# Performance work log

Measured on AMD Instinct MI355X. Metric: run time of the kernel, lower is better.

## Reference

```python
import jax, jax.numpy as jnp
import numpy as np

B, K, N, D, L = 16, 16, 1024, 256, 8
LN_EPS = 1e-5


def setup_inputs() -> dict:
    key = jax.random.key(0)
    ks = jax.random.split(key, 12)
    w = lambda k, sh: jax.random.normal(k, sh, jnp.float32) * 0.02
    return {
        "H": jax.random.normal(ks[0], (B, K, N, D), jnp.float32),
        "eps": jax.random.normal(ks[1], (B, L, D), jnp.float32),  # single Gaussian draw per batch
        "mu": jnp.zeros((1, L, D), jnp.float32),
        "log_sigma": jnp.full((1, L, D), -2.0, jnp.float32),
        "Wq": w(ks[2], (D, D)), "bq": jnp.zeros((D,), jnp.float32),
        "Wk": w(ks[3], (D, D)), "bk": jnp.zeros((D,), jnp.float32),
        "Wv": w(ks[4], (D, D)), "bv": jnp.zeros((D,), jnp.float32),
        "W_ih": w(ks[5], (3 * D, D)), "b_ih": jnp.zeros((3 * D,), jnp.float32),
        "W_hh": w(ks[6], (3 * D, D)), "b_hh": jnp.zeros((3 * D,), jnp.float32),
        "W1": w(ks[7], (D, D)), "b1": jnp.zeros((D,), jnp.float32),
        "W2": w(ks[8], (D, D)), "b2": jnp.zeros((D,), jnp.float32),
        "ln_g": jnp.ones((D,), jnp.float32), "ln_b": jnp.zeros((D,), jnp.float32),
    }


def reference(H, eps, mu, log_sigma, Wq, bq, Wk, bk, Wv, bv,
              W_ih, b_ih, W_hh, b_hh, W1, b1, W2, b2, ln_g, ln_b):
    d = H.shape[-1]
    scale = 1.0 / jnp.sqrt(jnp.asarray(d, H.dtype))
    slots0 = mu + jnp.exp(log_sigma) * eps  # [B,L,D]

    def step(slots, h_t):  # slots [B,L,D], h_t [B,N,D]
        Q = slots @ Wq.T + bq
        Kt = h_t @ Wk.T + bk
        V = h_t @ Wv.T + bv
        scores = jnp.einsum("bld,bnd->bln", Q, Kt) * scale
        attn = jnp.nan_to_num(jax.nn.softmax(scores, axis=-1))
        upd = jnp.einsum("bln,bnd->bld", attn, V)
        # torch.nn.GRUCell(input=upd, hidden=slots)
        gi = upd @ W_ih.T + b_ih
        gh = slots @ W_hh.T + b_hh
        ir, iz, inn = jnp.split(gi, 3, axis=-1)
        hr, hz, hn = jnp.split(gh, 3, axis=-1)
        r = jax.nn.sigmoid(ir + hr)
        z = jax.nn.sigmoid(iz + hz)
        n = jnp.tanh(inn + r * hn)
        s2 = (1.0 - z) * n + z * slots
        # FFN + residual + LayerNorm
        ffn = jnp.maximum(s2 @ W1.T + b1, 0.0) @ W2.T + b2
        x = s2 + ffn
        mean = x.mean(axis=-1, keepdims=True)
        var = x.var(axis=-1, keepdims=True)
        s3 = (x - mean) / jnp.sqrt(var + LN_EPS) * ln_g + ln_b
        return s3, (s3, attn)

    _, (S, Beta) = jax.lax.scan(step, slots0, jnp.swapaxes(H, 0, 1))
    return jnp.swapaxes(S, 0, 1), jnp.swapaxes(Beta, 0, 1)  # [B,K,L,D], [B,K,L,N]
```

## Files before the change

### kernel.cpp

```cpp
#include <hip/hip_runtime.h>
#include <math.h>


#define Bn 16
#define KK 16
#define Nn 1024
#define Dn 256
#define Ln 8

#define OFF_WQK   0
#define OFF_BQK   65536
#define OFF_WGIT  65792
#define OFF_BGI   262400
#define OFF_WHHT  263168
#define OFF_W1T   459776
#define OFF_W2T   525312
#define OFF_SLOTS 590848
#define OFF_QK    623616
#define OFF_PAV   656384
#define OFF_PDEN  1704960

__device__ __forceinline__ float sigmoidf_(float x) { return 1.f / (1.f + __expf(-x)); }

__global__ __launch_bounds__(256) void p1_kernel(
    const float* __restrict__ Wq, const float* __restrict__ bq,
    const float* __restrict__ Wk, float* __restrict__ Wqk, float* __restrict__ bqk) {
  int w = blockIdx.x, tid = threadIdx.x;
  if (w < 256) {
    float acc = 0.f;
    for (int a = 0; a < 256; ++a) acc += Wq[a * 256 + w] * Wk[a * 256 + tid];
    Wqk[w * 256 + tid] = acc;
  } else {
    float acc = 0.f;
    for (int a = 0; a < 256; ++a) acc += bq[a] * Wk[a * 256 + tid];
    bqk[tid] = acc;
  }
}

__global__ __launch_bounds__(256) void p2_kernel(
    const float* __restrict__ Wih, const float* __restrict__ bih,
    const float* __restrict__ Wv, const float* __restrict__ bv,
    float* __restrict__ WgiT, float* __restrict__ bgi) {
  int d = blockIdx.x, tid = threadIdx.x;
  float a0 = 0.f, a1 = 0.f, a2 = 0.f;
  for (int c = 0; c < 256; ++c) {
    float wv = Wv[c * 256 + d];
    a0 += Wih[tid * 256 + c] * wv;
    a1 += Wih[(tid + 256) * 256 + c] * wv;
    a2 += Wih[(tid + 512) * 256 + c] * wv;
  }
  WgiT[d * 768 + tid] = a0;
  WgiT[d * 768 + 256 + tid] = a1;
  WgiT[d * 768 + 512 + tid] = a2;
  if (d < 3) {
    int jj = d * 256 + tid;
    float s = bih[jj];
    for (int c = 0; c < 256; ++c) s += Wih[jj * 256 + c] * bv[c];
    bgi[jj] = s;
  }
}

__global__ __launch_bounds__(256) void p3_kernel(
    const float* __restrict__ Whh, const float* __restrict__ W1,
    const float* __restrict__ W2, float* __restrict__ WhhT,
    float* __restrict__ W1T, float* __restrict__ W2T) {
  __shared__ float tile[32][33];
  int wg = blockIdx.x, tid = threadIdx.x;
  const float* in; float* out; int R, C, tr, tc;
  if (wg < 192)      { in = Whh; out = WhhT; R = 768; C = 256; wg -= 0;   tr = wg >> 3; tc = wg & 7; }
  else if (wg < 256) { in = W1;  out = W1T;  R = 256; C = 256; wg -= 192; tr = wg >> 3; tc = wg & 7; }
  else               { in = W2;  out = W2T;  R = 256; C = 256; wg -= 256; tr = wg >> 3; tc = wg & 7; }
  int r = tid >> 5, c = tid & 31;
#pragma unroll
  for (int k = 0; k < 4; ++k)
    tile[r + 8 * k][c] = in[(tr * 32 + r + 8 * k) * C + tc * 32 + c];
  __syncthreads();
#pragma unroll
  for (int k = 0; k < 4; ++k)
    out[(tc * 32 + r + 8 * k) * R + tr * 32 + c] = tile[c][r + 8 * k];
}

__global__ __launch_bounds__(256) void init_slots_kernel(
    const float* __restrict__ eps, const float* __restrict__ mu,
    const float* __restrict__ lsig, float* __restrict__ slots) {
  int idx = blockIdx.x * 256 + threadIdx.x;
  int r = idx & 2047;
  slots[idx] = mu[r] + expf(lsig[r]) * eps[idx];
}

__global__ __launch_bounds__(256) void qk0_kernel(
    const float* __restrict__ Wqk, const float* __restrict__ bqk,
    const float* __restrict__ slots, float* __restrict__ Qkout) {
  __shared__ float sl_s[2048];
  int j = blockIdx.x & 7, b = blockIdx.x >> 3, tid = threadIdx.x;
  for (int k = 0; k < 8; ++k) sl_s[tid + k * 256] = slots[b * 2048 + tid + k * 256];
  __syncthreads();
  int l = tid >> 5, ee = j * 32 + (tid & 31);
  float acc = bqk[ee];
  for (int d = 0; d < 256; ++d) acc += sl_s[l * 256 + d] * Wqk[d * 256 + ee];
  Qkout[b * 2048 + l * 256 + ee] = acc;
}

__global__ __launch_bounds__(256) void attn_kernel(
    const float* __restrict__ H, const float* __restrict__ Qk,
    float* __restrict__ beta_out, float* __restrict__ par_av,
    float* __restrict__ par_den, int t) {
  __shared__ float h_s[32 * 258];
  __shared__ float qk_s[Ln * Dn];
  __shared__ float e_s[256];
  __shared__ float red[256];
  int tile = blockIdx.x, b = blockIdx.y, tid = threadIdx.x;
#pragma unroll
  for (int k = 0; k < 8; ++k) qk_s[tid + k * 256] = Qk[b * 2048 + tid + k * 256];
  const float* Hbase = H + (((long)b * KK + t) * Nn + tile * 32) * Dn;
  const float4* src = (const float4*)Hbase;
#pragma unroll
  for (int k = 0; k < 8; ++k) {
    int idx4 = tid + k * 256;
    int r = idx4 >> 6, d4 = idx4 & 63;
    float4 v = src[idx4];
    float* dst = &h_s[r * 258 + d4 * 4];
    ((float2*)dst)[0] = make_float2(v.x, v.y);
    ((float2*)dst)[1] = make_float2(v.z, v.w);
  }
  __syncthreads();
  int l = tid >> 5, row = tid & 31;
  {
    const float2* hr2 = (const float2*)(&h_s[row * 258]);
    const float2* qr2 = (const float2*)(&qk_s[l * 256]);
    float acc = 0.f;
#pragma unroll 8
    for (int e = 0; e < 128; ++e) {
      float2 hv = hr2[e], qv = qr2[e];
      acc += hv.x * qv.x + hv.y * qv.y;
    }
    float ev = __expf(acc * 0.0625f);
    e_s[tid] = ev;
    red[tid] = ev;
    beta_out[(((long)b * KK + t) * Ln + l) * Nn + tile * 32 + row] = ev;
  }
  __syncthreads();
  if (tid < 8) {
    float s = 0.f;
    for (int i = 0; i < 32; ++i) s += red[tid * 32 + i];
    par_den[(b * 32 + tile) * 8 + tid] = s;
  }
  float av[8];
#pragma unroll
  for (int i = 0; i < 8; ++i) av[i] = 0.f;
  for (int rr = 0; rr < 32; ++rr) {
    float hv = h_s[rr * 258 + tid];
#pragma unroll
    for (int i = 0; i < 8; ++i) av[i] += e_s[i * 32 + rr] * hv;
  }
  long pbase = (long)(b * 32 + tile) * 2048;
#pragma unroll
  for (int i = 0; i < 8; ++i) par_av[pbase + i * 256 + tid] = av[i];
}

__global__ __launch_bounds__(1024) void chain_kernel(
    const float* __restrict__ WgiT, const float* __restrict__ bgi,
    const float* __restrict__ WhhT, const float* __restrict__ bhh,
    const float* __restrict__ W1T, const float* __restrict__ b1,
    const float* __restrict__ W2T, const float* __restrict__ b2,
    const float* __restrict__ Wqk, const float* __restrict__ bqk,
    const float* __restrict__ ln_g, const float* __restrict__ ln_b,
    const float* __restrict__ par_av, const float* __restrict__ par_den,
    float* __restrict__ slots, float* __restrict__ S, float* __restrict__ Beta,
    float* __restrict__ Qk, int t) {
  __shared__ float upd_s[256], sl_s[256], s2_s[256], f_s[256], s3_s[256];
  __shared__ float red6[6][4][256];
  __shared__ float den_inv;
  __shared__ float lnred[8];
  int b = blockIdx.x >> 3, l = blockIdx.x & 7;
  int tid = threadIdx.x, kc = tid >> 8, c = tid & 255;

  {
    float ps = 0.f;
    long pvb = (long)(b * 32) * 2048 + l * 256 + c;
#pragma unroll
    for (int i = 0; i < 8; ++i) ps += par_av[pvb + (long)(kc * 8 + i) * 2048];
    red6[0][kc][c] = ps;
    float dv = 0.f;
    if (tid < 64) {
      if (tid < 32) dv = par_den[(b * 32 + tid) * 8 + l];
#pragma unroll
      for (int m = 1; m < 64; m <<= 1) dv += __shfl_xor(dv, m);
      if (tid == 0) den_inv = 1.f / dv;
    }
    if (kc == 1) sl_s[c] = slots[b * 2048 + l * 256 + c];
  }
  __syncthreads();
  float rd = den_inv;
  if (kc == 0)
    upd_s[c] = (red6[0][0][c] + red6[0][1][c] + red6[0][2][c] + red6[0][3][c]) * rd;
  {
    long bb = (((long)b * KK + t) * Ln + l) * Nn;
    Beta[bb + tid] *= rd;
  }
  __syncthreads();

  {
    float ir = 0, iz = 0, in_ = 0, hr = 0, hz = 0, hn = 0;
#pragma unroll 4
    for (int i = 0; i < 64; ++i) {
      int e = kc * 64 + i;
      float u = upd_s[e], s = sl_s[e];
      const float* wg = WgiT + (long)e * 768;
      const float* wh = WhhT + (long)e * 768;
      ir += u * wg[c];       iz += u * wg[256 + c];  in_ += u * wg[512 + c];
      hr += s * wh[c];       hz += s * wh[256 + c];  hn  += s * wh[512 + c];
    }
    red6[0][kc][c] = ir; red6[1][kc][c] = iz; red6[2][kc][c] = in_;
    red6[3][kc][c] = hr; red6[4][kc][c] = hz; red6[5][kc][c] = hn;
  }
  __syncthreads();
  if (kc == 0) {
    float tir = red6[0][0][c] + red6[0][1][c] + red6[0][2][c] + red6[0][3][c] + bgi[c];
    float tiz = red6[1][0][c] + red6[1][1][c] + red6[1][2][c] + red6[1][3][c] + bgi[256 + c];
    float tin = red6[2][0][c] + red6[2][1][c] + red6[2][2][c] + red6[2][3][c] + bgi[512 + c];
    float thr = red6[3][0][c] + red6[3][1][c] + red6[3][2][c] + red6[3][3][c] + bhh[c];
    float thz = red6[4][0][c] + red6[4][1][c] + red6[4][2][c] + red6[4][3][c] + bhh[256 + c];
    float thn = red6[5][0][c] + red6[5][1][c] + red6[5][2][c] + red6[5][3][c] + bhh[512 + c];
    float r = sigmoidf_(tir + thr);
    float z = sigmoidf_(tiz + thz);
    float n = tanhf(tin + r * thn);
    s2_s[c] = (1.f - z) * n + z * sl_s[c];
  }
  __syncthreads();

  {
    float f = 0.f;
#pragma unroll 4
    for (int i = 0; i < 64; ++i) {
      int e = kc * 64 + i;
      f += s2_s[e] * W1T[e * 256 + c];
    }
    red6[0][kc][c] = f;
  }
  __syncthreads();
  if (kc == 0)
    f_s[c] = fmaxf(red6[0][0][c] + red6[0][1][c] + red6[0][2][c] + red6[0][3][c] + b1[c], 0.f);
  __syncthreads();

  {
    float x = 0.f;
#pragma unroll 4
    for (int i = 0; i < 64; ++i) {
      int e = kc * 64 + i;
      x += f_s[e] * W2T[e * 256 + c];
    }
    red6[1][kc][c] = x;
  }
  __syncthreads();
  float xv = 0.f;
  if (kc == 0) {
    xv = red6[1][0][c] + red6[1][1][c] + red6[1][2][c] + red6[1][3][c] + b2[c] + s2_s[c];
    float sr = xv, qr = xv * xv;
#pragma unroll
    for (int m = 1; m < 64; m <<= 1) {
      sr += __shfl_xor(sr, m);
      qr += __shfl_xor(qr, m);
    }
    if ((c & 63) == 0) { lnred[c >> 6] = sr; lnred[4 + (c >> 6)] = qr; }
  }
  __syncthreads();
  if (kc == 0) {
    float m = (lnred[0] + lnred[1] + lnred[2] + lnred[3]) * (1.f / 256.f);
    float v = (lnred[4] + lnred[5] + lnred[6] + lnred[7]) * (1.f / 256.f) - m * m;
    float s3 = (xv - m) * rsqrtf(v + 1e-5f) * ln_g[c] + ln_b[c];
    s3_s[c] = s3;
    S[(((long)b * KK + t) * Ln + l) * Dn + c] = s3;
    slots[b * 2048 + l * 256 + c] = s3;
  }
  __syncthreads();

  {
    float q = 0.f;
#pragma unroll 4
    for (int i = 0; i < 64; ++i) {
      int e = kc * 64 + i;
      q += s3_s[e] * Wqk[e * 256 + c];
    }
    red6[0][kc][c] = q;
  }
  __syncthreads();
  if (kc == 0)
    Qk[b * 2048 + l * 256 + c] =
        red6[0][0][c] + red6[0][1][c] + red6[0][2][c] + red6[0][3][c] + bqk[c];
}

extern "C" void kernel_launch(void* const* d_in, const int* in_sizes, int n_in,
                              void* d_out, int out_size, void* d_ws, size_t ws_size,
                              hipStream_t stream) {
  const float* H    = (const float*)d_in[0];
  const float* eps  = (const float*)d_in[1];
  const float* mu   = (const float*)d_in[2];
  const float* lsig = (const float*)d_in[3];
  const float* Wq   = (const float*)d_in[4];
  const float* bq   = (const float*)d_in[5];
  const float* Wk   = (const float*)d_in[6];
  const float* Wv   = (const float*)d_in[8];
  const float* bv   = (const float*)d_in[9];
  const float* Wih  = (const float*)d_in[10];
  const float* bih  = (const float*)d_in[11];
  const float* Whh  = (const float*)d_in[12];
  const float* bhh  = (const float*)d_in[13];
  const float* W1   = (const float*)d_in[14];
  const float* b1   = (const float*)d_in[15];
  const float* W2   = (const float*)d_in[16];
  const float* b2   = (const float*)d_in[17];
  const float* ln_g = (const float*)d_in[18];
  const float* ln_b = (const float*)d_in[19];

  float* out = (float*)d_out;
  float* S    = out;
  float* Beta = out + (long)Bn * KK * Ln * Dn;

  float* ws = (float*)d_ws;
  float* Wqk   = ws + OFF_WQK;
  float* bqk   = ws + OFF_BQK;
  float* WgiT  = ws + OFF_WGIT;
  float* bgi   = ws + OFF_BGI;
  float* WhhT  = ws + OFF_WHHT;
  float* W1T   = ws + OFF_W1T;
  float* W2T   = ws + OFF_W2T;
  float* slots = ws + OFF_SLOTS;
  float* Qk    = ws + OFF_QK;
  float* pav   = ws + OFF_PAV;
  float* pden  = ws + OFF_PDEN;

  p1_kernel<<<257, 256, 0, stream>>>(Wq, bq, Wk, Wqk, bqk);
  p2_kernel<<<256, 256, 0, stream>>>(Wih, bih, Wv, bv, WgiT, bgi);
  p3_kernel<<<320, 256, 0, stream>>>(Whh, W1, W2, WhhT, W1T, W2T);
  init_slots_kernel<<<128, 256, 0, stream>>>(eps, mu, lsig, slots);
  qk0_kernel<<<128, 256, 0, stream>>>(Wqk, bqk, slots, Qk);

  for (int t = 0; t < KK; ++t) {
    attn_kernel<<<dim3(32, 16), 256, 0, stream>>>(H, Qk, Beta, pav, pden, t);
    chain_kernel<<<128, 1024, 0, stream>>>(WgiT, bgi, WhhT, bhh, W1T, b1, W2T, b2,
                                           Wqk, bqk, ln_g, ln_b, pav, pden,
                                           slots, S, Beta, Qk, t);
  }
}
```

Baseline: 1.063 ms.

## Split GRU gate matmuls into a separate K-split kernel reusing weights across slots

The per-step chain kernel is split in two. A new gru_kernel runs 256 blocks, each holding a 16-row K-chunk of WgiT and WhhT in shared memory, and computes partial gate products for all 8 slots of a batch, so each weight chunk is read once per batch rather than once per slot. A slimmer chain2 kernel then sums the 16 partials and does the activations, FFN, LayerNorm and Qk projection. This removes the redundant global weight traffic of the 128-block chain kernel, at the cost of an extra launch per step and a partial-sum buffer round trip through global memory.

```diff
diff --git a/kernel.cpp b/kernel.cpp
--- a/kernel.cpp
+++ b/kernel.cpp
@@ -19,6 +19,7 @@
 #define OFF_QK    623616
 #define OFF_PAV   656384
 #define OFF_PDEN  1704960
+#define OFF_PG    1709056
 
 __device__ __forceinline__ float sigmoidf_(float x) { return 1.f / (1.f + __expf(-x)); }
 
@@ -158,64 +159,127 @@
   for (int i = 0; i < 8; ++i) par_av[pbase + i * 256 + tid] = av[i];
 }
 
-__global__ __launch_bounds__(1024) void chain_kernel(
-    const float* __restrict__ WgiT, const float* __restrict__ bgi,
-    const float* __restrict__ WhhT, const float* __restrict__ bhh,
+__global__ __launch_bounds__(1024) void gru_kernel(
+    const float* __restrict__ WgiT, const float* __restrict__ WhhT,
+    const float* __restrict__ par_av, const float* __restrict__ par_den,
+    const float* __restrict__ slots, float* __restrict__ Beta,
+    float* __restrict__ pg, int t) {
+  __shared__ float w_s[16 * 768];
+  __shared__ float rupd[8][128];
+  __shared__ float upd_s[128];
+  __shared__ float sl_s[128];
+  __shared__ float den_s[8];
+  int b = blockIdx.x >> 4, kc = blockIdx.x & 15;
+  int tid = threadIdx.x;
+
+  const float4* wsrc = (const float4*)(WgiT + kc * 12288);
+  float4 wv0 = wsrc[tid], wv1 = wsrc[tid + 1024], wv2 = wsrc[tid + 2048];
+  {
+    int g = tid >> 7, le = tid & 127;
+    int l = le >> 4, e = le & 15;
+    float ps = 0.f;
+    long base = ((long)(b * 32)) * 2048 + l * 256 + kc * 16 + e;
+#pragma unroll
+    for (int i = 0; i < 4; ++i) ps += par_av[base + (long)(g * 4 + i) * 2048];
+    rupd[g][le] = ps;
+  }
+  if (tid < 256) {
+    int ll = tid >> 5, tl = tid & 31;
+    float dv = par_den[(b * 32 + tl) * 8 + ll];
+#pragma unroll
+    for (int m = 1; m < 32; m <<= 1) dv += __shfl_xor(dv, m);
+    if (tl == 0) den_s[ll] = 1.f / dv;
+  }
+  if (tid < 128) sl_s[tid] = slots[b * 2048 + (tid >> 4) * 256 + kc * 16 + (tid & 15)];
+  ((float4*)w_s)[tid] = wv0;
+  ((float4*)w_s)[tid + 1024] = wv1;
+  ((float4*)w_s)[tid + 2048] = wv2;
+  __syncthreads();
+
+  if (tid < 512) {
+    int idx = kc * 512 + tid;
+    Beta[(((long)b * KK + t) * Ln) * Nn + idx] *= den_s[idx >> 10];
+  }
+  if (tid < 128) {
+    float s = 0.f;
+#pragma unroll
+    for (int g = 0; g < 8; ++g) s += rupd[g][tid];
+    upd_s[tid] = s * den_s[tid >> 4];
+  }
+  __syncthreads();
+
+  int l4 = tid >> 8, cb = tid & 255;
+  long pb0 = ((long)(b * 16 + kc) * 8 + l4) * 1536;
+  long pb1 = ((long)(b * 16 + kc) * 8 + l4 + 4) * 1536;
+  {
+    float a0 = 0.f, a1 = 0.f, a2 = 0.f, a3 = 0.f, a4 = 0.f, a5 = 0.f;
+#pragma unroll
+    for (int e = 0; e < 16; ++e) {
+      float u0 = upd_s[l4 * 16 + e];
+      float u1 = upd_s[(l4 + 4) * 16 + e];
+      float w0 = w_s[e * 768 + cb];
+      float w1 = w_s[e * 768 + 256 + cb];
+      float w2 = w_s[e * 768 + 512 + cb];
+      a0 += u0 * w0; a1 += u0 * w1; a2 += u0 * w2;
+      a3 += u1 * w0; a4 += u1 * w1; a5 += u1 * w2;
+    }
+    pg[pb0 + cb] = a0; pg[pb0 + 256 + cb] = a1; pg[pb0 + 512 + cb] = a2;
+    pg[pb1 + cb] = a3; pg[pb1 + 256 + cb] = a4; pg[pb1 + 512 + cb] = a5;
+  }
+  __syncthreads();
+  {
+    const float4* hsrc = (const float4*)(WhhT + kc * 12288);
+    ((float4*)w_s)[tid] = hsrc[tid];
+    ((float4*)w_s)[tid + 1024] = hsrc[tid + 1024];
+    ((float4*)w_s)[tid + 2048] = hsrc[tid + 2048];
+  }
+  __syncthreads();
+  {
+    float a0 = 0.f, a1 = 0.f, a2 = 0.f, a3 = 0.f, a4 = 0.f, a5 = 0.f;
+#pragma unroll
+    for (int e = 0; e < 16; ++e) {
+      float s0 = sl_s[l4 * 16 + e];
+      float s1 = sl_s[(l4 + 4) * 16 + e];
+      float w0 = w_s[e * 768 + cb];
+      float w1 = w_s[e * 768 + 256 + cb];
+      float w2 = w_s[e * 768 + 512 + cb];
+      a0 += s0 * w0; a1 += s0 * w1; a2 += s0 * w2;
+      a3 += s1 * w0; a4 += s1 * w1; a5 += s1 * w2;
+    }
+    pg[pb0 + 768 + cb] = a0; pg[pb0 + 1024 + cb] = a1; pg[pb0 + 1280 + cb] = a2;
+    pg[pb1 + 768 + cb] = a3; pg[pb1 + 1024 + cb] = a4; pg[pb1 + 1280 + cb] = a5;
+  }
+}
+
+__global__ __launch_bounds__(1024) void chain2_kernel(
+    const float* __restrict__ pg, const float* __restrict__ bgi,
+    const float* __restrict__ bhh,
     const float* __restrict__ W1T, const float* __restrict__ b1,
     const float* __restrict__ W2T, const float* __restrict__ b2,
     const float* __restrict__ Wqk, const float* __restrict__ bqk,
     const float* __restrict__ ln_g, const float* __restrict__ ln_b,
-    const float* __restrict__ par_av, const float* __restrict__ par_den,
-    float* __restrict__ slots, float* __restrict__ S, float* __restrict__ Beta,
-    float* __restrict__ Qk, int t) {
-  __shared__ float upd_s[256], sl_s[256], s2_s[256], f_s[256], s3_s[256];
+    float* __restrict__ slots, float* __restrict__ S, float* __restrict__ Qk,
+    int t) {
+  __shared__ float sl_s[256], s2_s[256], f_s[256], s3_s[256];
   __shared__ float red6[6][4][256];
-  __shared__ float den_inv;
   __shared__ float lnred[8];
   int b = blockIdx.x >> 3, l = blockIdx.x & 7;
-  int tid = threadIdx.x, kc = tid >> 8, c = tid & 255;
-
-  {
-    float ps = 0.f;
-    long pvb = (long)(b * 32) * 2048 + l * 256 + c;
-#pragma unroll
-    for (int i = 0; i < 8; ++i) ps += par_av[pvb + (long)(kc * 8 + i) * 2048];
-    red6[0][kc][c] = ps;
-    float dv = 0.f;
-    if (tid < 64) {
-      if (tid < 32) dv = par_den[(b * 32 + tid) * 8 + l];
-#pragma unroll
-      for (int m = 1; m < 64; m <<= 1) dv += __shfl_xor(dv, m);
-      if (tid == 0) den_inv = 1.f / dv;
-    }
-    if (kc == 1) sl_s[c] = slots[b * 2048 + l * 256 + c];
-  }
-  __syncthreads();
-  float rd = den_inv;
-  if (kc == 0)
-    upd_s[c] = (red6[0][0][c] + red6[0][1][c] + red6[0][2][c] + red6[0][3][c]) * rd;
-  {
-    long bb = (((long)b * KK + t) * Ln + l) * Nn;
-    Beta[bb + tid] *= rd;
-  }
-  __syncthreads();
-
+  int tid = threadIdx.x, q = tid >> 8, c = tid & 255;
+
+  if (tid < 256) sl_s[tid] = slots[b * 2048 + l * 256 + tid];
   {
     float ir = 0, iz = 0, in_ = 0, hr = 0, hz = 0, hn = 0;
-#pragma unroll 4
-    for (int i = 0; i < 64; ++i) {
-      int e = kc * 64 + i;
-      float u = upd_s[e], s = sl_s[e];
-      const float* wg = WgiT + (long)e * 768;
-      const float* wh = WhhT + (long)e * 768;
-      ir += u * wg[c];       iz += u * wg[256 + c];  in_ += u * wg[512 + c];
-      hr += s * wh[c];       hz += s * wh[256 + c];  hn  += s * wh[512 + c];
-    }
-    red6[0][kc][c] = ir; red6[1][kc][c] = iz; red6[2][kc][c] = in_;
-    red6[3][kc][c] = hr; red6[4][kc][c] = hz; red6[5][kc][c] = hn;
-  }
-  __syncthreads();
-  if (kc == 0) {
+#pragma unroll
+    for (int j = 0; j < 4; ++j) {
+      const float* p = pg + ((long)(b * 16 + q * 4 + j) * 8 + l) * 1536;
+      ir += p[c];        iz += p[256 + c];   in_ += p[512 + c];
+      hr += p[768 + c];  hz += p[1024 + c];  hn  += p[1280 + c];
+    }
+    red6[0][q][c] = ir; red6[1][q][c] = iz; red6[2][q][c] = in_;
+    red6[3][q][c] = hr; red6[4][q][c] = hz; red6[5][q][c] = hn;
+  }
+  __syncthreads();
+  if (q == 0) {
     float tir = red6[0][0][c] + red6[0][1][c] + red6[0][2][c] + red6[0][3][c] + bgi[c];
     float tiz = red6[1][0][c] + red6[1][1][c] + red6[1][2][c] + red6[1][3][c] + bgi[256 + c];
     float tin = red6[2][0][c] + red6[2][1][c] + red6[2][2][c] + red6[2][3][c] + bgi[512 + c];
@@ -233,13 +297,13 @@
     float f = 0.f;
 #pragma unroll 4
     for (int i = 0; i < 64; ++i) {
-      int e = kc * 64 + i;
+      int e = q * 64 + i;
       f += s2_s[e] * W1T[e * 256 + c];
     }
-    red6[0][kc][c] = f;
-  }
-  __syncthreads();
-  if (kc == 0)
+    red6[0][q][c] = f;
+  }
+  __syncthreads();
+  if (q == 0)
     f_s[c] = fmaxf(red6[0][0][c] + red6[0][1][c] + red6[0][2][c] + red6[0][3][c] + b1[c], 0.f);
   __syncthreads();
 
@@ -247,14 +311,14 @@
     float x = 0.f;
 #pragma unroll 4
     for (int i = 0; i < 64; ++i) {
-      int e = kc * 64 + i;
+      int e = q * 64 + i;
       x += f_s[e] * W2T[e * 256 + c];
     }
-    red6[1][kc][c] = x;
+    red6[1][q][c] = x;
   }
   __syncthreads();
   float xv = 0.f;
-  if (kc == 0) {
+  if (q == 0) {
     xv = red6[1][0][c] + red6[1][1][c] + red6[1][2][c] + red6[1][3][c] + b2[c] + s2_s[c];
     float sr = xv, qr = xv * xv;
 #pragma unroll
@@ -265,7 +329,7 @@
     if ((c & 63) == 0) { lnred[c >> 6] = sr; lnred[4 + (c >> 6)] = qr; }
   }
   __syncthreads();
-  if (kc == 0) {
+  if (q == 0) {
     float m = (lnred[0] + lnred[1] + lnred[2] + lnred[3]) * (1.f / 256.f);
     float v = (lnred[4] + lnred[5] + lnred[6] + lnred[7]) * (1.f / 256.f) - m * m;
     float s3 = (xv - m) * rsqrtf(v + 1e-5f) * ln_g[c] + ln_b[c];
@@ -276,16 +340,16 @@
   __syncthreads();
 
   {
-    float q = 0.f;
+    float qacc = 0.f;
 #pragma unroll 4
     for (int i = 0; i < 64; ++i) {
-      int e = kc * 64 + i;
-      q += s3_s[e] * Wqk[e * 256 + c];
-    }
-    red6[0][kc][c] = q;
-  }
-  __syncthreads();
-  if (kc == 0)
+      int e = q * 64 + i;
+      qacc += s3_s[e] * Wqk[e * 256 + c];
+    }
+    red6[0][q][c] = qacc;
+  }
+  __syncthreads();
+  if (q == 0)
     Qk[b * 2048 + l * 256 + c] =
         red6[0][0][c] + red6[0][1][c] + red6[0][2][c] + red6[0][3][c] + bqk[c];
 }
@@ -329,6 +393,7 @@
   float* Qk    = ws + OFF_QK;
   float* pav   = ws + OFF_PAV;
   float* pden  = ws + OFF_PDEN;
+  float* pg    = ws + OFF_PG;
 
   p1_kernel<<<257, 256, 0, stream>>>(Wq, bq, Wk, Wqk, bqk);
   p2_kernel<<<256, 256, 0, stream>>>(Wih, bih, Wv, bv, WgiT, bgi);
@@ -338,8 +403,8 @@
 
   for (int t = 0; t < KK; ++t) {
     attn_kernel<<<dim3(32, 16), 256, 0, stream>>>(H, Qk, Beta, pav, pden, t);
-    chain_kernel<<<128, 1024, 0, stream>>>(WgiT, bgi, WhhT, bhh, W1T, b1, W2T, b2,
-                                           Wqk, bqk, ln_g, ln_b, pav, pden,
-                                           slots, S, Beta, Qk, t);
-  }
-}
+    gru_kernel<<<256, 1024, 0, stream>>>(WgiT, WhhT, pav, pden, slots, Beta, pg, t);
+    chain2_kernel<<<128, 1024, 0, stream>>>(pg, bgi, bhh, W1T, b1, W2T, b2,
+                                            Wqk, bqk, ln_g, ln_b, slots, S, Qk, t);
+  }
+}
```

Result: faster. 1.017 ms (-4.3%).

## Fuse recurrent time loop into one persistent kernel with software grid barriers

Applied to the files above, without the earlier changes.

Replaces the 32 per-timestep attention and chain launches with a single persistent kernel of 256 workgroups that loops over all 16 timesteps, separated by atomic-counter grid barriers. Each workgroup keeps its slice of the GRU input and hidden weights resident in shared memory, and the GRU, FFN and LayerNorm work is split column-wise across all workgroups instead of 128 blocks. The aim is to remove launch overhead and the per-step reload of weights. The cost is four grid-wide syncs per step, and the design relies on all 256 workgroups being co-resident to avoid deadlock.

```diff
diff --git a/kernel.cpp b/kernel.cpp
--- a/kernel.cpp
+++ b/kernel.cpp
@@ -7,18 +7,22 @@
 #define Nn 1024
 #define Dn 256
 #define Ln 8
+#define NWG 256u
 
 #define OFF_WQK   0
 #define OFF_BQK   65536
 #define OFF_WGIT  65792
 #define OFF_BGI   262400
-#define OFF_WHHT  263168
-#define OFF_W1T   459776
-#define OFF_W2T   525312
-#define OFF_SLOTS 590848
-#define OFF_QK    623616
-#define OFF_PAV   656384
-#define OFF_PDEN  1704960
+#define OFF_W2T   263168
+#define OFF_WGIR  328704
+#define OFF_WHHR  525312
+#define OFF_SLOTS 721920
+#define OFF_QK    754688
+#define OFF_PAV   787456
+#define OFF_PDEN  1311744
+#define OFF_S2G   1313792
+#define OFF_PX    1346560
+#define OFF_BAR   1870848
 
 __device__ __forceinline__ float sigmoidf_(float x) { return 1.f / (1.f + __expf(-x)); }
 
@@ -60,30 +64,54 @@
   }
 }
 
-__global__ __launch_bounds__(256) void p3_kernel(
-    const float* __restrict__ Whh, const float* __restrict__ W1,
-    const float* __restrict__ W2, float* __restrict__ WhhT,
-    float* __restrict__ W1T, float* __restrict__ W2T) {
-  __shared__ float tile[32][33];
+__global__ __launch_bounds__(256) void p2b_kernel(
+    const float* __restrict__ WgiT, const float* __restrict__ Whh,
+    const float* __restrict__ W2,
+    float* __restrict__ Wgi_r, float* __restrict__ Whh_r, float* __restrict__ W2T) {
+  __shared__ float tile[48 * 257];
   int wg = blockIdx.x, tid = threadIdx.x;
-  const float* in; float* out; int R, C, tr, tc;
-  if (wg < 192)      { in = Whh; out = WhhT; R = 768; C = 256; wg -= 0;   tr = wg >> 3; tc = wg & 7; }
-  else if (wg < 256) { in = W1;  out = W1T;  R = 256; C = 256; wg -= 192; tr = wg >> 3; tc = wg & 7; }
-  else               { in = W2;  out = W2T;  R = 256; C = 256; wg -= 256; tr = wg >> 3; tc = wg & 7; }
-  int r = tid >> 5, c = tid & 31;
-#pragma unroll
-  for (int k = 0; k < 4; ++k)
-    tile[r + 8 * k][c] = in[(tr * 32 + r + 8 * k) * C + tc * 32 + c];
-  __syncthreads();
-#pragma unroll
-  for (int k = 0; k < 4; ++k)
-    out[(tc * 32 + r + 8 * k) * R + tr * 32 + c] = tile[c][r + 8 * k];
+  if (wg < 16) {
+    int j = wg, col = tid & 63, e0 = tid >> 6;
+    if (col < 48) {
+      int g = col >> 4, cl = col & 15;
+      for (int eb = 0; eb < 64; ++eb) {
+        int e = eb * 4 + e0;
+        Wgi_r[j * 12288 + e * 48 + col] = WgiT[e * 768 + g * 256 + 16 * j + cl];
+      }
+    }
+  } else if (wg < 32) {
+    int j = wg - 16;
+    for (int r = 0; r < 48; ++r) {
+      int grow = (r >> 4) * 256 + 16 * j + (r & 15);
+      tile[r * 257 + tid] = Whh[grow * 256 + tid];
+    }
+    __syncthreads();
+    int rr = tid & 63, e0 = tid >> 6;
+    if (rr < 48) {
+      for (int eb = 0; eb < 64; ++eb) {
+        int e = eb * 4 + e0;
+        Whh_r[j * 12288 + e * 48 + rr] = tile[rr * 257 + e];
+      }
+    }
+  } else {
+    int w2 = wg - 32, tr = w2 >> 3, tc = w2 & 7;
+    int r = tid >> 5, c = tid & 31;
+#pragma unroll
+    for (int k = 0; k < 4; ++k)
+      tile[(r + 8 * k) * 33 + c] = W2[(tr * 32 + r + 8 * k) * 256 + tc * 32 + c];
+    __syncthreads();
+#pragma unroll
+    for (int k = 0; k < 4; ++k)
+      W2T[(tc * 32 + r + 8 * k) * 256 + tr * 32 + c] = tile[c * 33 + (r + 8 * k)];
+  }
 }
 
 __global__ __launch_bounds__(256) void init_slots_kernel(
     const float* __restrict__ eps, const float* __restrict__ mu,
-    const float* __restrict__ lsig, float* __restrict__ slots) {
+    const float* __restrict__ lsig, float* __restrict__ slots,
+    unsigned* __restrict__ bar) {
   int idx = blockIdx.x * 256 + threadIdx.x;
+  if (idx < 2) bar[idx] = 0u;
   int r = idx & 2047;
   slots[idx] = mu[r] + expf(lsig[r]) * eps[idx];
 }
@@ -101,193 +129,296 @@
   Qkout[b * 2048 + l * 256 + ee] = acc;
 }
 
-__global__ __launch_bounds__(256) void attn_kernel(
-    const float* __restrict__ H, const float* __restrict__ Qk,
-    float* __restrict__ beta_out, float* __restrict__ par_av,
-    float* __restrict__ par_den, int t) {
-  __shared__ float h_s[32 * 258];
-  __shared__ float qk_s[Ln * Dn];
-  __shared__ float e_s[256];
-  __shared__ float red[256];
-  int tile = blockIdx.x, b = blockIdx.y, tid = threadIdx.x;
-#pragma unroll
-  for (int k = 0; k < 8; ++k) qk_s[tid + k * 256] = Qk[b * 2048 + tid + k * 256];
-  const float* Hbase = H + (((long)b * KK + t) * Nn + tile * 32) * Dn;
-  const float4* src = (const float4*)Hbase;
-#pragma unroll
-  for (int k = 0; k < 8; ++k) {
-    int idx4 = tid + k * 256;
-    int r = idx4 >> 6, d4 = idx4 & 63;
-    float4 v = src[idx4];
-    float* dst = &h_s[r * 258 + d4 * 4];
-    ((float2*)dst)[0] = make_float2(v.x, v.y);
-    ((float2*)dst)[1] = make_float2(v.z, v.w);
-  }
+__device__ __forceinline__ void grid_sync(unsigned* cnt, unsigned* gen, unsigned round) {
   __syncthreads();
-  int l = tid >> 5, row = tid & 31;
-  {
-    const float2* hr2 = (const float2*)(&h_s[row * 258]);
-    const float2* qr2 = (const float2*)(&qk_s[l * 256]);
-    float acc = 0.f;
-#pragma unroll 8
-    for (int e = 0; e < 128; ++e) {
-      float2 hv = hr2[e], qv = qr2[e];
-      acc += hv.x * qv.x + hv.y * qv.y;
-    }
-    float ev = __expf(acc * 0.0625f);
-    e_s[tid] = ev;
-    red[tid] = ev;
-    beta_out[(((long)b * KK + t) * Ln + l) * Nn + tile * 32 + row] = ev;
+  if (threadIdx.x == 0) {
+    __threadfence();
+    unsigned prev = __hip_atomic_fetch_add(cnt, 1u, __ATOMIC_RELAXED, __HIP_MEMORY_SCOPE_AGENT);
+    if (prev == round * NWG - 1u) {
+      __hip_atomic_store(gen, round, __ATOMIC_RELAXED, __HIP_MEMORY_SCOPE_AGENT);
+    } else {
+      unsigned g;
+      do {
+        __builtin_amdgcn_s_sleep(2);
+        g = __hip_atomic_load(gen, __ATOMIC_RELAXED, __HIP_MEMORY_SCOPE_AGENT);
+      } while (g < round);
+    }
+    __threadfence();
   }
   __syncthreads();
-  if (tid < 8) {
-    float s = 0.f;
-    for (int i = 0; i < 32; ++i) s += red[tid * 32 + i];
-    par_den[(b * 32 + tile) * 8 + tid] = s;
-  }
-  float av[8];
-#pragma unroll
-  for (int i = 0; i < 8; ++i) av[i] = 0.f;
-  for (int rr = 0; rr < 32; ++rr) {
-    float hv = h_s[rr * 258 + tid];
-#pragma unroll
-    for (int i = 0; i < 8; ++i) av[i] += e_s[i * 32 + rr] * hv;
-  }
-  long pbase = (long)(b * 32 + tile) * 2048;
-#pragma unroll
-  for (int i = 0; i < 8; ++i) par_av[pbase + i * 256 + tid] = av[i];
-}
-
-__global__ __launch_bounds__(1024) void chain_kernel(
-    const float* __restrict__ WgiT, const float* __restrict__ bgi,
-    const float* __restrict__ WhhT, const float* __restrict__ bhh,
-    const float* __restrict__ W1T, const float* __restrict__ b1,
+}
+
+__global__ __launch_bounds__(1024, 4) void fused_kernel(
+    const float* __restrict__ H,
+    const float* __restrict__ Wgi_r, const float* __restrict__ bgi,
+    const float* __restrict__ Whh_r, const float* __restrict__ bhh,
+    const float* __restrict__ W1, const float* __restrict__ b1,
     const float* __restrict__ W2T, const float* __restrict__ b2,
     const float* __restrict__ Wqk, const float* __restrict__ bqk,
     const float* __restrict__ ln_g, const float* __restrict__ ln_b,
-    const float* __restrict__ par_av, const float* __restrict__ par_den,
-    float* __restrict__ slots, float* __restrict__ S, float* __restrict__ Beta,
-    float* __restrict__ Qk, int t) {
-  __shared__ float upd_s[256], sl_s[256], s2_s[256], f_s[256], s3_s[256];
-  __shared__ float red6[6][4][256];
-  __shared__ float den_inv;
-  __shared__ float lnred[8];
-  int b = blockIdx.x >> 3, l = blockIdx.x & 7;
-  int tid = threadIdx.x, kc = tid >> 8, c = tid & 255;
+    float* __restrict__ slots, float* __restrict__ QkG,
+    float* __restrict__ S, float* __restrict__ Beta,
+    float* __restrict__ pav, float* __restrict__ pden,
+    float* __restrict__ s2g, float* __restrict__ px,
+    unsigned* __restrict__ bar) {
+  __shared__ float smem[32256];
+  float* wgic = smem;
+  float* whhc = smem + 12288;
+  float* scratch = smem + 24576;
+
+  int wid = blockIdx.x;
+  int xcd = wid & 7, slot = wid >> 3;
+  int b = xcd * 2 + (slot >> 4), j = slot & 15;
+  int tid = threadIdx.x;
 
   {
-    float ps = 0.f;
-    long pvb = (long)(b * 32) * 2048 + l * 256 + c;
-#pragma unroll
-    for (int i = 0; i < 8; ++i) ps += par_av[pvb + (long)(kc * 8 + i) * 2048];
-    red6[0][kc][c] = ps;
-    float dv = 0.f;
-    if (tid < 64) {
-      if (tid < 32) dv = par_den[(b * 32 + tid) * 8 + l];
-#pragma unroll
-      for (int m = 1; m < 64; m <<= 1) dv += __shfl_xor(dv, m);
-      if (tid == 0) den_inv = 1.f / dv;
-    }
-    if (kc == 1) sl_s[c] = slots[b * 2048 + l * 256 + c];
-  }
+    const float4* gsrc = (const float4*)(Wgi_r + j * 12288);
+    const float4* hsrc = (const float4*)(Whh_r + j * 12288);
+    float4* gdst = (float4*)wgic;
+    float4* hdst = (float4*)whhc;
+    for (int i = tid; i < 3072; i += 1024) { gdst[i] = gsrc[i]; hdst[i] = hsrc[i]; }
+  }
+  unsigned* cnt = bar;
+  unsigned* gen = bar + 1;
+  unsigned rnd = 0;
   __syncthreads();
-  float rd = den_inv;
-  if (kc == 0)
-    upd_s[c] = (red6[0][0][c] + red6[0][1][c] + red6[0][2][c] + red6[0][3][c]) * rd;
-  {
-    long bb = (((long)b * KK + t) * Ln + l) * Nn;
-    Beta[bb + tid] *= rd;
-  }
-  __syncthreads();
-
-  {
-    float ir = 0, iz = 0, in_ = 0, hr = 0, hz = 0, hn = 0;
-#pragma unroll 4
-    for (int i = 0; i < 64; ++i) {
-      int e = kc * 64 + i;
-      float u = upd_s[e], s = sl_s[e];
-      const float* wg = WgiT + (long)e * 768;
-      const float* wh = WhhT + (long)e * 768;
-      ir += u * wg[c];       iz += u * wg[256 + c];  in_ += u * wg[512 + c];
-      hr += s * wh[c];       hz += s * wh[256 + c];  hn  += s * wh[512 + c];
-    }
-    red6[0][kc][c] = ir; red6[1][kc][c] = iz; red6[2][kc][c] = in_;
-    red6[3][kc][c] = hr; red6[4][kc][c] = hz; red6[5][kc][c] = hn;
-  }
-  __syncthreads();
-  if (kc == 0) {
-    float tir = red6[0][0][c] + red6[0][1][c] + red6[0][2][c] + red6[0][3][c] + bgi[c];
-    float tiz = red6[1][0][c] + red6[1][1][c] + red6[1][2][c] + red6[1][3][c] + bgi[256 + c];
-    float tin = red6[2][0][c] + red6[2][1][c] + red6[2][2][c] + red6[2][3][c] + bgi[512 + c];
-    float thr = red6[3][0][c] + red6[3][1][c] + red6[3][2][c] + red6[3][3][c] + bhh[c];
-    float thz = red6[4][0][c] + red6[4][1][c] + red6[4][2][c] + red6[4][3][c] + bhh[256 + c];
-    float thn = red6[5][0][c] + red6[5][1][c] + red6[5][2][c] + red6[5][3][c] + bhh[512 + c];
-    float r = sigmoidf_(tir + thr);
-    float z = sigmoidf_(tiz + thz);
-    float n = tanhf(tin + r * thn);
-    s2_s[c] = (1.f - z) * n + z * sl_s[c];
-  }
-  __syncthreads();
-
-  {
-    float f = 0.f;
-#pragma unroll 4
-    for (int i = 0; i < 64; ++i) {
-      int e = kc * 64 + i;
-      f += s2_s[e] * W1T[e * 256 + c];
-    }
-    red6[0][kc][c] = f;
-  }
-  __syncthreads();
-  if (kc == 0)
-    f_s[c] = fmaxf(red6[0][0][c] + red6[0][1][c] + red6[0][2][c] + red6[0][3][c] + b1[c], 0.f);
-  __syncthreads();
-
-  {
-    float x = 0.f;
-#pragma unroll 4
-    for (int i = 0; i < 64; ++i) {
-      int e = kc * 64 + i;
-      x += f_s[e] * W2T[e * 256 + c];
-    }
-    red6[1][kc][c] = x;
-  }
-  __syncthreads();
-  float xv = 0.f;
-  if (kc == 0) {
-    xv = red6[1][0][c] + red6[1][1][c] + red6[1][2][c] + red6[1][3][c] + b2[c] + s2_s[c];
-    float sr = xv, qr = xv * xv;
-#pragma unroll
-    for (int m = 1; m < 64; m <<= 1) {
-      sr += __shfl_xor(sr, m);
-      qr += __shfl_xor(qr, m);
-    }
-    if ((c & 63) == 0) { lnred[c >> 6] = sr; lnred[4 + (c >> 6)] = qr; }
-  }
-  __syncthreads();
-  if (kc == 0) {
-    float m = (lnred[0] + lnred[1] + lnred[2] + lnred[3]) * (1.f / 256.f);
-    float v = (lnred[4] + lnred[5] + lnred[6] + lnred[7]) * (1.f / 256.f) - m * m;
-    float s3 = (xv - m) * rsqrtf(v + 1e-5f) * ln_g[c] + ln_b[c];
-    s3_s[c] = s3;
-    S[(((long)b * KK + t) * Ln + l) * Dn + c] = s3;
-    slots[b * 2048 + l * 256 + c] = s3;
-  }
-  __syncthreads();
-
-  {
-    float q = 0.f;
-#pragma unroll 4
-    for (int i = 0; i < 64; ++i) {
-      int e = kc * 64 + i;
-      q += s3_s[e] * Wqk[e * 256 + c];
-    }
-    red6[0][kc][c] = q;
-  }
-  __syncthreads();
-  if (kc == 0)
-    Qk[b * 2048 + l * 256 + c] =
-        red6[0][0][c] + red6[0][1][c] + red6[0][2][c] + red6[0][3][c] + bqk[c];
+
+  for (int t = 0; t < KK; ++t) {
+    {
+      float* hs = scratch;
+      float* es = scratch + 4160;
+      float* avred = scratch + 4672;
+      float acc8[8];
+#pragma unroll
+      for (int i = 0; i < 8; ++i) acc8[i] = 0.f;
+      const float* Hb = H + (((long)(b * 16) + t) * 1024 + j * 64) * 256;
+      const float* Qkb = QkG + b * 2048;
+      for (int st = 0; st < 4; ++st) {
+        __syncthreads();
+        {
+          const float4* src = (const float4*)(Hb + st * 4096);
+          int r = tid >> 6, d4 = tid & 63;
+          float4 v = src[tid];
+          float* dst = &hs[r * 260 + d4 * 4];
+          ((float2*)dst)[0] = make_float2(v.x, v.y);
+          ((float2*)dst)[1] = make_float2(v.z, v.w);
+        }
+        __syncthreads();
+        {
+          int wv = tid >> 6, lane = tid & 63, l = lane >> 3, e8 = lane & 7;
+          const float4* hr = (const float4*)(&hs[wv * 260 + e8 * 32]);
+          const float4* qr = (const float4*)(Qkb + l * 256 + e8 * 32);
+          float a = 0.f;
+#pragma unroll
+          for (int i = 0; i < 8; ++i) {
+            float4 hv = hr[i], qv = qr[i];
+            a += hv.x * qv.x + hv.y * qv.y + hv.z * qv.z + hv.w * qv.w;
+          }
+          a += __shfl_xor(a, 1); a += __shfl_xor(a, 2); a += __shfl_xor(a, 4);
+          if (e8 == 0) es[(st * 16 + wv) * 8 + l] = __expf(a * 0.0625f);
+        }
+        __syncthreads();
+        {
+          int g = tid >> 8, d = tid & 255;
+#pragma unroll
+          for (int rr = 0; rr < 4; ++rr) {
+            int r = g * 4 + rr;
+            float hv = hs[r * 260 + d];
+            const float4* ep = (const float4*)(&es[(st * 16 + r) * 8]);
+            float4 e0 = ep[0], e1 = ep[1];
+            acc8[0] += e0.x * hv; acc8[1] += e0.y * hv;
+            acc8[2] += e0.z * hv; acc8[3] += e0.w * hv;
+            acc8[4] += e1.x * hv; acc8[5] += e1.y * hv;
+            acc8[6] += e1.z * hv; acc8[7] += e1.w * hv;
+          }
+        }
+      }
+      __syncthreads();
+      if (tid < 512) {
+        int l = tid >> 6, r = tid & 63;
+        Beta[(((long)(b * 16) + t) * 8 + l) * 1024 + j * 64 + r] = es[r * 8 + l];
+      }
+      if (tid < 64) {
+        int l = tid >> 3, ch = tid & 7;
+        float s = 0.f;
+#pragma unroll
+        for (int i = 0; i < 8; ++i) s += es[(ch * 8 + i) * 8 + l];
+        s += __shfl_xor(s, 1); s += __shfl_xor(s, 2); s += __shfl_xor(s, 4);
+        if (ch == 0) pden[(b * 16 + j) * 8 + l] = s;
+      }
+      for (int g2 = 0; g2 < 4; ++g2) {
+        if ((tid >> 8) == g2) {
+          int d = tid & 255;
+#pragma unroll
+          for (int l = 0; l < 8; ++l) {
+            if (g2 == 0) avred[l * 256 + d] = acc8[l];
+            else avred[l * 256 + d] += acc8[l];
+          }
+        }
+        __syncthreads();
+      }
+      for (int s = tid; s < 2048; s += 1024)
+        pav[(long)(b * 16 + j) * 2048 + s] = avred[s];
+    }
+    grid_sync(cnt, gen, ++rnd);
+
+    {
+      float* upd = scratch;
+      float* sls = scratch + 2048;
+      float* gsum = scratch + 4096;
+      float* dens = scratch + 4864;
+      if (tid < 8) {
+        float s = 0.f;
+        for (int jj = 0; jj < 16; ++jj) s += pden[(b * 16 + jj) * 8 + tid];
+        dens[tid] = 1.f / s;
+      }
+      sls[tid] = slots[b * 2048 + tid];
+      sls[tid + 1024] = slots[b * 2048 + tid + 1024];
+      __syncthreads();
+      for (int s = tid; s < 2048; s += 1024) {
+        int l = s >> 8;
+        float a = 0.f;
+#pragma unroll
+        for (int jj = 0; jj < 16; ++jj) a += pav[(long)(b * 16 + jj) * 2048 + s];
+        upd[s] = a * dens[l];
+      }
+      if (tid < 512) {
+        int l = tid >> 6, r = tid & 63;
+        long o = (((long)(b * 16) + t) * 8 + l) * 1024 + j * 64 + r;
+        Beta[o] *= dens[l];
+      }
+      __syncthreads();
+      if (tid < 384) {
+        int gh6 = tid >> 6, l2 = (tid >> 4) & 3, cl = tid & 15;
+        bool isg = gh6 < 3;
+        int g = isg ? gh6 : gh6 - 3;
+        const float* wb = (isg ? wgic : whhc) + g * 16 + cl;
+        const float* x0 = (isg ? upd : sls) + l2 * 256;
+        const float* x1 = x0 + 1024;
+        float a0 = 0.f, a1 = 0.f;
+#pragma unroll 8
+        for (int e = 0; e < 256; ++e) {
+          float w = wb[e * 48];
+          a0 += x0[e] * w;
+          a1 += x1[e] * w;
+        }
+        float bias = isg ? bgi[g * 256 + 16 * j + cl] : bhh[g * 256 + 16 * j + cl];
+        gsum[gh6 * 128 + l2 * 16 + cl] = a0 + bias;
+        gsum[gh6 * 128 + (l2 + 4) * 16 + cl] = a1 + bias;
+      }
+      __syncthreads();
+      if (tid < 128) {
+        int l = tid >> 4, cl = tid & 15;
+        float r = sigmoidf_(gsum[tid] + gsum[384 + tid]);
+        float z = sigmoidf_(gsum[128 + tid] + gsum[512 + tid]);
+        float n = tanhf(gsum[256 + tid] + r * gsum[640 + tid]);
+        float s2 = (1.f - z) * n + z * sls[l * 256 + 16 * j + cl];
+        s2g[b * 2048 + l * 256 + 16 * j + cl] = s2;
+      }
+    }
+    grid_sync(cnt, gen, ++rnd);
+
+    {
+      float* wbuf = scratch;
+      float* s2f = scratch + 4352;
+      float* red8 = scratch + 6400;
+      float* f1s = scratch + 7552;
+      {
+        int e = tid & 255, c4 = tid >> 8;
+#pragma unroll
+        for (int i = 0; i < 4; ++i) {
+          int cl = c4 * 4 + i;
+          wbuf[e * 17 + cl] = W1[(16 * j + cl) * 256 + e];
+        }
+      }
+      for (int s = tid; s < 2048; s += 1024) s2f[s] = s2g[b * 2048 + s];
+      __syncthreads();
+      {
+        int q = tid >> 7, p = tid & 127, l = p >> 4, cl = p & 15;
+        const float* xp = s2f + l * 256 + q * 32;
+        const float* wp = wbuf + (q * 32) * 17 + cl;
+        float a = 0.f;
+#pragma unroll 8
+        for (int e = 0; e < 32; ++e) a += xp[e] * wp[e * 17];
+        red8[p * 9 + q] = a;
+      }
+      __syncthreads();
+      float f1v = 0.f;
+      if (tid < 128) {
+        float a = b1[16 * j + (tid & 15)];
+#pragma unroll
+        for (int q = 0; q < 8; ++q) a += red8[tid * 9 + q];
+        f1v = fmaxf(a, 0.f);
+      }
+      for (int s = tid; s < 4096; s += 1024) {
+        int e = s >> 8, cout = s & 255;
+        wbuf[e * 256 + cout] = W2T[(16 * j + e) * 256 + cout];
+      }
+      if (tid < 128) f1s[tid] = f1v;
+      __syncthreads();
+      {
+        int lh = tid >> 8, cout = tid & 255;
+#pragma unroll
+        for (int li = 0; li < 2; ++li) {
+          int l = lh + li * 4;
+          float a = 0.f;
+#pragma unroll
+          for (int e = 0; e < 16; ++e) a += f1s[l * 16 + e] * wbuf[e * 256 + cout];
+          px[((long)(b * 16 + j) * 8 + l) * 256 + cout] = a;
+        }
+      }
+    }
+    grid_sync(cnt, gen, ++rnd);
+
+    if (j < 8) {
+      int l = j;
+      float* red4 = scratch;
+      float* xrow = scratch + 1024;
+      float* s3f = scratch + 1280;
+      float* lnr = scratch + 1536;
+      {
+        int q = tid >> 8, cout = tid & 255;
+        float a = 0.f;
+#pragma unroll
+        for (int jj = 0; jj < 4; ++jj)
+          a += px[((long)(b * 16 + q * 4 + jj) * 8 + l) * 256 + cout];
+        red4[q * 256 + cout] = a;
+      }
+      __syncthreads();
+      if (tid < 256) {
+        float x = red4[tid] + red4[256 + tid] + red4[512 + tid] + red4[768 + tid]
+                + b2[tid] + s2g[b * 2048 + l * 256 + tid];
+        xrow[tid] = x;
+        float sr = x, qr = x * x;
+#pragma unroll
+        for (int m = 1; m < 64; m <<= 1) { sr += __shfl_xor(sr, m); qr += __shfl_xor(qr, m); }
+        if ((tid & 63) == 0) { lnr[tid >> 6] = sr; lnr[4 + (tid >> 6)] = qr; }
+      }
+      __syncthreads();
+      if (tid < 256) {
+        float m = (lnr[0] + lnr[1] + lnr[2] + lnr[3]) * (1.f / 256.f);
+        float v = (lnr[4] + lnr[5] + lnr[6] + lnr[7]) * (1.f / 256.f) - m * m;
+        float s3 = (xrow[tid] - m) * rsqrtf(v + 1e-5f) * ln_g[tid] + ln_b[tid];
+        s3f[tid] = s3;
+        S[(((long)(b * 16) + t) * 8 + l) * 256 + tid] = s3;
+        slots[b * 2048 + l * 256 + tid] = s3;
+      }
+      __syncthreads();
+      {
+        int q = tid >> 8, cout = tid & 255;
+        const float* wq = Wqk + q * 64 * 256 + cout;
+        float a = 0.f;
+#pragma unroll 8
+        for (int e = 0; e < 64; ++e) a += s3f[q * 64 + e] * wq[e * 256];
+        red4[q * 256 + cout] = a;
+      }
+      __syncthreads();
+      if (tid < 256)
+        QkG[b * 2048 + l * 256 + tid] =
+            red4[tid] + red4[256 + tid] + red4[512 + tid] + red4[768 + tid] + bqk[tid];
+    }
+    grid_sync(cnt, gen, ++rnd);
+  }
 }
 
 extern "C" void kernel_launch(void* const* d_in, const int* in_sizes, int n_in,
@@ -322,24 +453,24 @@
   float* bqk   = ws + OFF_BQK;
   float* WgiT  = ws + OFF_WGIT;
   float* bgi   = ws + OFF_BGI;
-  float* WhhT  = ws + OFF_WHHT;
-  float* W1T   = ws + OFF_W1T;
   float* W2T   = ws + OFF_W2T;
+  float* Wgi_r = ws + OFF_WGIR;
+  float* Whh_r = ws + OFF_WHHR;
   float* slots = ws + OFF_SLOTS;
   float* Qk    = ws + OFF_QK;
   float* pav   = ws + OFF_PAV;
   float* pden  = ws + OFF_PDEN;
+  float* s2g   = ws + OFF_S2G;
+  float* px    = ws + OFF_PX;
+  unsigned* bar = (unsigned*)(ws + OFF_BAR);
 
   p1_kernel<<<257, 256, 0, stream>>>(Wq, bq, Wk, Wqk, bqk);
   p2_kernel<<<256, 256, 0, stream>>>(Wih, bih, Wv, bv, WgiT, bgi);
-  p3_kernel<<<320, 256, 0, stream>>>(Whh, W1, W2, WhhT, W1T, W2T);
-  init_slots_kernel<<<128, 256, 0, stream>>>(eps, mu, lsig, slots);
+  p2b_kernel<<<96, 256, 0, stream>>>(WgiT, Whh, W2, Wgi_r, Whh_r, W2T);
+  init_slots_kernel<<<128, 256, 0, stream>>>(eps, mu, lsig, slots, bar);
   qk0_kernel<<<128, 256, 0, stream>>>(Wqk, bqk, slots, Qk);
 
-  for (int t = 0; t < KK; ++t) {
-    attn_kernel<<<dim3(32, 16), 256, 0, stream>>>(H, Qk, Beta, pav, pden, t);
-    chain_kernel<<<128, 1024, 0, stream>>>(WgiT, bgi, WhhT, bhh, W1T, b1, W2T, b2,
-                                           Wqk, bqk, ln_g, ln_b, pav, pden,
-                                           slots, S, Beta, Qk, t);
-  }
-}
+  fused_kernel<<<256, 1024, 0, stream>>>(
+      H, Wgi_r, bgi, Whh_r, bhh, W1, b1, W2T, b2, Wqk, bqk, ln_g, ln_b,
+      slots, Qk, S, Beta, pav, pden, s2g, px, bar);
+}
```

Result: slower. 3.039 ms (+185.9%).
